# Optimization experiments

Measured on AMD Instinct MI355X. Metric: run time of the kernel, lower is better.

Reference implementation:

```python
import jax, jax.numpy as jnp
import numpy as np

N_NODES = 20000
N_EDGES = 50000
IN_DIM = 128
HID = 128
OUT_DIM = 64
N_PAIRS = 128
N_LAYERS = 2
N_HEADS = 4


def setup_inputs() -> dict:
    key = jax.random.key(0)
    ks = jax.random.split(key, 32)
    s = 0.05
    def p(k, shape):
        return jax.random.normal(k, shape, jnp.float32) * s
    inp = {}
    inp["node_features"] = jax.random.normal(ks[0], (N_NODES, IN_DIM), jnp.float32)
    inp["edge_index"] = jax.random.randint(ks[1], (2, N_EDGES), 0, N_NODES, jnp.int32)
    inp["edge_timestamps"] = jax.random.uniform(ks[2], (N_EDGES,), jnp.float32)
    inp["target_pairs"] = jax.random.randint(ks[3], (N_PAIRS, 2), 0, N_NODES, jnp.int32)
    inp["in_W"] = p(ks[4], (HID, IN_DIM)); inp["in_b"] = p(ks[5], (HID,))
    inp["te_W1"] = p(ks[6], (N_LAYERS, HID, 1)); inp["te_b1"] = p(ks[7], (N_LAYERS, HID))
    inp["te_W2"] = p(ks[8], (N_LAYERS, HID, HID)); inp["te_b2"] = p(ks[9], (N_LAYERS, HID))
    inp["attn_in_W"] = p(ks[10], (N_LAYERS, 3 * HID, HID)); inp["attn_in_b"] = p(ks[11], (N_LAYERS, 3 * HID))
    inp["attn_out_W"] = p(ks[12], (N_LAYERS, HID, HID)); inp["attn_out_b"] = p(ks[13], (N_LAYERS, HID))
    inp["ft_W"] = p(ks[14], (N_LAYERS, HID, HID)); inp["ft_b"] = p(ks[15], (N_LAYERS, HID))
    inp["op_W"] = p(ks[16], (N_LAYERS, HID, HID)); inp["op_b"] = p(ks[17], (N_LAYERS, HID))
    inp["out1_W"] = p(ks[18], (HID, HID)); inp["out1_b"] = p(ks[19], (HID,))
    inp["out2_W"] = p(ks[20], (OUT_DIM, HID)); inp["out2_b"] = p(ks[21], (OUT_DIM,))
    inp["lp1_W"] = p(ks[22], (HID, 2 * OUT_DIM)); inp["lp1_b"] = p(ks[23], (HID,))
    inp["lp2_W"] = p(ks[24], (HID // 2, HID)); inp["lp2_b"] = p(ks[25], (HID // 2,))
    inp["lp3_W"] = p(ks[26], (1, HID // 2)); inp["lp3_b"] = p(ks[27], (1,))
    return inp


def _forward(node_features, edge_index, edge_timestamps, target_pairs,
             in_W, in_b, te_W1, te_b1, te_W2, te_b2,
             attn_in_W, attn_in_b, attn_out_W, attn_out_b,
             ft_W, ft_b, op_W, op_b,
             out1_W, out1_b, out2_W, out2_b,
             lp1_W, lp1_b, lp2_W, lp2_b, lp3_W, lp3_b):
    N = node_features.shape[0]
    h = in_W.shape[0]
    H = N_HEADS
    d = h // H
    scale = 1.0 / np.sqrt(d).astype(np.float32)
    src, dst = edge_index[0], edge_index[1]
    # flattened target nodes; duplicates compute identical rows so dedup (torch.unique) is unneeded
    targets = target_pairs.reshape(-1)  # [U]
    U = targets.shape[0]
    E = src.shape[0]

    x = node_features @ in_W.T + in_b  # [N, h]
    for l in range(te_W1.shape[0]):
        tf = x @ ft_W[l].T + ft_b[l]                                           # [N, h]
        tfeat = jax.nn.relu(edge_timestamps[:, None] @ te_W1[l].T + te_b1[l])
        tfeat = tfeat @ te_W2[l].T + te_b2[l]                                  # [E, h]
        Wq, Wk, Wv = jnp.split(attn_in_W[l], 3, axis=0)
        bq, bk, bv = jnp.split(attn_in_b[l], 3)
        q = (tf[targets] @ Wq.T + bq).reshape(U, H, d)
        # keys/values are linear in (tf[nbr] + tfeat): split into node term A and edge term B
        Ak = (tf @ Wk.T).reshape(N, H, d)
        Bk = (tfeat @ Wk.T + bk).reshape(E, H, d)
        Av = (tf @ Wv.T).reshape(N, H, d)
        Bv = (tfeat @ Wv.T + bv).reshape(E, H, d)
        is_src = src[None, :] == targets[:, None]          # [U, E]
        mask = is_src | (dst[None, :] == targets[:, None])  # edge incident to target
        nbr = jnp.where(is_src, dst[None, :], src[None, :])  # other endpoint, [U, E]
        qAk = jnp.einsum('uhd,nhd->uhn', q, Ak) * scale      # [U, H, N]
        idx = jnp.broadcast_to(nbr[:, None, :], (U, H, E))
        s_node = jnp.take_along_axis(qAk, idx, axis=2)        # [U, H, E]
        s_edge = jnp.einsum('uhd,ehd->uhe', q, Bk) * scale
        scores = jnp.where(mask[:, None, :], s_node + s_edge, -1e30)
        p = jax.nn.softmax(scores, axis=-1)
        p = jnp.where(mask[:, None, :], p, 0.0)               # [U, H, E]
        out_edge = jnp.einsum('uhe,ehd->uhd', p, Bv)
        # sum_e p * Av[nbr] via per-target scatter of probs into node space
        w = jax.vmap(lambda pe, ne: jax.ops.segment_sum(pe, ne, num_segments=N))(
            p.transpose(0, 2, 1), nbr)                        # [U, N, H]
        out_node = jnp.einsum('unh,nhd->uhd', w, Av)
        attn = (out_node + out_edge).reshape(U, h) @ attn_out_W[l].T + attn_out_b[l]
        has_nbr = mask.any(axis=1)
        agg_in = jnp.where(has_nbr[:, None], attn, tf[targets])
        agg = agg_in @ op_W[l].T + op_b[l]
        x = x.at[targets].set(agg)
        x = jax.nn.relu(x)
    emb = jax.nn.relu(x @ out1_W.T + out1_b) @ out2_W.T + out2_b  # [N, out]
    pair = jnp.concatenate([emb[target_pairs[:, 0]], emb[target_pairs[:, 1]]], axis=1)
    z = jax.nn.relu(pair @ lp1_W.T + lp1_b)
    z = jax.nn.relu(z @ lp2_W.T + lp2_b)
    return jax.nn.sigmoid(z @ lp3_W.T + lp3_b)  # [B, 1]


def reference(node_features, edge_index, edge_timestamps, target_pairs,
              in_W, in_b, te_W1, te_b1, te_W2, te_b2,
              attn_in_W, attn_in_b, attn_out_W, attn_out_b,
              ft_W, ft_b, op_W, op_b,
              out1_W, out1_b, out2_W, out2_b,
              lp1_W, lp1_b, lp2_W, lp2_b, lp3_W, lp3_b):
    return _forward(node_features, edge_index, edge_timestamps, target_pairs,
                    in_W, in_b, te_W1, te_b1, te_W2, te_b2,
                    attn_in_W, attn_in_b, attn_out_W, attn_out_b,
                    ft_W, ft_b, op_W, op_b,
                    out1_W, out1_b, out2_W, out2_b,
                    lp1_W, lp1_b, lp2_W, lp2_b, lp3_W, lp3_b)
```

## Files before the change

kernel.cpp:

```cpp
#include <hip/hip_runtime.h>
#include <math.h>

#define N_NODES 20000
#define N_EDGES 50000
#define N_SLOTS 256
#define N_PAIRS 128
#define CAP 32
#define MSTRIDE 16384
#define NMAT 19
#define TFLAG (1 << 30)
#define HSZ 1024
#define NBLK 256
#define BATCH 16

__device__ __forceinline__ float4 relu4(float4 v) {
    return make_float4(fmaxf(v.x, 0.f), fmaxf(v.y, 0.f), fmaxf(v.z, 0.f), fmaxf(v.w, 0.f));
}
__device__ __forceinline__ float4 add4(float4 a, float4 b) {
    return make_float4(a.x + b.x, a.y + b.y, a.z + b.z, a.w + b.w);
}
__device__ __forceinline__ void fma4(float4& acc, const float4 w, const float s) {
    acc.x = fmaf(w.x, s, acc.x); acc.y = fmaf(w.y, s, acc.y);
    acc.z = fmaf(w.z, s, acc.z); acc.w = fmaf(w.w, s, acc.w);
}
#define F4Z make_float4(0.f, 0.f, 0.f, 0.f)

__device__ __forceinline__ void gbar(unsigned* cnt, unsigned target, bool wait) {
    __syncthreads();
    if (threadIdx.x == 0) {
        __builtin_amdgcn_fence(__ATOMIC_RELEASE, "agent");
        __hip_atomic_fetch_add(cnt, 1u, __ATOMIC_RELAXED, __HIP_MEMORY_SCOPE_AGENT);
        if (wait) {
            int it = 0;
            while (true) {
                unsigned v;
                if ((it++ & 7) != 7)
                    v = __hip_atomic_load(cnt, __ATOMIC_RELAXED,
                                          __HIP_MEMORY_SCOPE_SYSTEM);
                else
                    v = __hip_atomic_fetch_add(cnt, 0u, __ATOMIC_RELAXED,
                                               __HIP_MEMORY_SCOPE_AGENT);
                if (v >= target) break;
                __builtin_amdgcn_s_sleep(16);
            }
            __builtin_amdgcn_fence(__ATOMIC_ACQUIRE, "agent");
        }
    }
    __syncthreads();
}

__device__ __forceinline__ float4 mv_ks1_g8(const float* __restrict__ WT,
                                            const float* __restrict__ xv128,
                                            int g, int jj) {
    const float4* W4 = (const float4*)WT;
    const float4* x4 = (const float4*)xv128;
    float4 acc = F4Z;
#pragma unroll
    for (int kk4 = 0; kk4 < 4; ++kk4) {
        int k4 = g * 4 + kk4;
        float4 xv = x4[k4];
        fma4(acc, W4[(k4 * 4 + 0) * 32 + jj], xv.x);
        fma4(acc, W4[(k4 * 4 + 1) * 32 + jj], xv.y);
        fma4(acc, W4[(k4 * 4 + 2) * 32 + jj], xv.z);
        fma4(acc, W4[(k4 * 4 + 3) * 32 + jj], xv.w);
    }
    return acc;
}
__device__ __forceinline__ float4 mv_ks1_g8_64(const float* __restrict__ WT,
                                               const float* __restrict__ xv128,
                                               int g, int jj) {
    const float4* W4 = (const float4*)WT;
    const float4* x4 = (const float4*)xv128;
    int j16 = jj & 15;
    float4 acc = F4Z;
#pragma unroll
    for (int kk4 = 0; kk4 < 4; ++kk4) {
        int k4 = g * 4 + kk4;
        float4 xv = x4[k4];
        fma4(acc, W4[(k4 * 4 + 0) * 16 + j16], xv.x);
        fma4(acc, W4[(k4 * 4 + 1) * 16 + j16], xv.y);
        fma4(acc, W4[(k4 * 4 + 2) * 16 + j16], xv.z);
        fma4(acc, W4[(k4 * 4 + 3) * 16 + j16], xv.w);
    }
    return acc;
}
__device__ __forceinline__ float4 comb1_g8(const float4* pb, int jj) {
    float4 s = pb[jj];
#pragma unroll
    for (int gp = 1; gp < 8; ++gp) s = add4(s, pb[gp * 32 + jj]);
    return s;
}

__device__ __forceinline__ void mv16_g8(const float* __restrict__ WT,
                                        const float* __restrict__ xs,
                                        int g, int jj, float4* acc) {
    const float4* W4 = (const float4*)WT;
    const float4* x4 = (const float4*)xs;
#pragma unroll
    for (int kk4 = 0; kk4 < 4; ++kk4) {
        int k4 = g * 4 + kk4;
        float4 w0 = W4[(k4 * 4 + 0) * 32 + jj];
        float4 w1 = W4[(k4 * 4 + 1) * 32 + jj];
        float4 w2 = W4[(k4 * 4 + 2) * 32 + jj];
        float4 w3 = W4[(k4 * 4 + 3) * 32 + jj];
#pragma unroll
        for (int e = 0; e < 16; ++e) {
            float4 xv = x4[e * 32 + k4];
            fma4(acc[e], w0, xv.x); fma4(acc[e], w1, xv.y);
            fma4(acc[e], w2, xv.z); fma4(acc[e], w3, xv.w);
        }
    }
}
__device__ __forceinline__ float4 comb16_g8(const float4* pb, int it, int jj) {
    float4 s = pb[it * 32 + jj];
#pragma unroll
    for (int gp = 1; gp < 8; ++gp) s = add4(s, pb[(gp * 16 + it) * 32 + jj]);
    return s;
}

__device__ __forceinline__ float4 mv_ks1(const float* __restrict__ WT,
                                         const float* __restrict__ xv128,
                                         int g, int jj) {
    const float4* W4 = (const float4*)WT;
    const float4* x4 = (const float4*)xv128;
    float4 acc = F4Z;
#pragma unroll 2
    for (int kk4 = 0; kk4 < 8; ++kk4) {
        int k4 = g * 8 + kk4;
        float4 xv = x4[k4];
        fma4(acc, W4[(k4 * 4 + 0) * 32 + jj], xv.x);
        fma4(acc, W4[(k4 * 4 + 1) * 32 + jj], xv.y);
        fma4(acc, W4[(k4 * 4 + 2) * 32 + jj], xv.z);
        fma4(acc, W4[(k4 * 4 + 3) * 32 + jj], xv.w);
    }
    return acc;
}
__device__ __forceinline__ float4 mv_ks1_64(const float* __restrict__ WT,
                                            const float* __restrict__ xv128,
                                            int g, int jj) {
    const float4* W4 = (const float4*)WT;
    const float4* x4 = (const float4*)xv128;
    int j16 = jj & 15;
    float4 acc = F4Z;
#pragma unroll 2
    for (int kk4 = 0; kk4 < 8; ++kk4) {
        int k4 = g * 8 + kk4;
        float4 xv = x4[k4];
        fma4(acc, W4[(k4 * 4 + 0) * 16 + j16], xv.x);
        fma4(acc, W4[(k4 * 4 + 1) * 16 + j16], xv.y);
        fma4(acc, W4[(k4 * 4 + 2) * 16 + j16], xv.z);
        fma4(acc, W4[(k4 * 4 + 3) * 16 + j16], xv.w);
    }
    return acc;
}
__device__ __forceinline__ float4 comb1(const float4* pb, int jj) {
    return add4(add4(pb[jj], pb[32 + jj]), add4(pb[64 + jj], pb[96 + jj]));
}

__device__ __forceinline__ unsigned thash(int key) {
    return ((unsigned)key * 2654435761u) >> 22;
}
__device__ __forceinline__ bool hexists(const int* __restrict__ hkey, int key) {
    unsigned h = thash(key);
    while (true) {
        int k = hkey[h];
        if (k == -1) return false;
        if (k == key) return true;
        h = (h + 1) & (HSZ - 1);
    }
}
__device__ __forceinline__ void hemit_g(const int* __restrict__ hkey,
                                        const int* __restrict__ hval,
                                        int* __restrict__ gcnt,
                                        int2* __restrict__ lst,
                                        int key, int e, int nbrf) {
    unsigned h = thash(key);
    while (true) {
        int k = hkey[h];
        if (k == -1) return;
        if (k == key) {
            int s = hval[h];
            int pos = atomicAdd(&gcnt[s], 1);
            if (pos < CAP) lst[s * CAP + pos] = make_int2(e, nbrf);
        }
        h = (h + 1) & (HSZ - 1);
    }
}

struct Params {
    const float* nf; const int* ei; const float* ts; const int* tp;
    const float* inW; const float* inb;
    const float* teW1; const float* teb1; const float* teW2; const float* teb2;
    const float* aiW; const float* aib; const float* aoW; const float* aob;
    const float* ftW; const float* ftb; const float* opW; const float* opb;
    const float* o1W; const float* o1b; const float* o2W; const float* o2b;
    const float* l1W; const float* l1b; const float* l2W; const float* l2b;
    const float* l3W; const float* l3b;
    float* out; float* x; int* cnt; int2* lst; float* emb; float* WT;
    unsigned* bar; unsigned* flg;
};

__global__ __launch_bounds__(256, 1) void k_fused(Params P) {
    __shared__ __align__(16) float xu[128], x0u[128], tfv[128], qv[128], sv[128];
    __shared__ __align__(16) float xs[BATCH * 128], t1s[BATCH * 128];
    __shared__ __align__(16) float x0s[BATCH * 128];
    __shared__ __align__(16) float zs[CAP * 128];
    __shared__ __align__(16) float4 pb[8 * 16 * 32];
    __shared__ __align__(16) float qkh[4 * 128];
    __shared__ __align__(16) float zbl[4 * 128];
    __shared__ float scl[CAP * 4], ps[CAP * 4], sbk[4];
    __shared__ int nbr_s[BATCH], tf_s[BATCH];
    __shared__ float ts_s[BATCH];
    __shared__ __align__(16) float tile[32][129];
    __shared__ int hkey[HSZ], hval[HSZ];

    const int b = blockIdx.x, tid = threadIdx.x, g = tid >> 5, jj = tid & 31;

    if (b < 72) {
        int m, r0, rows;
        if (b < 68) { m = b >> 2; r0 = (b & 3) * 32; rows = 128; }
        else { int mm = b - 68; m = 17 + (mm >> 1); r0 = (mm & 1) * 32; rows = 64; }
        const float* src;
        if (m == 0) src = P.inW;
        else if (m <= 2) src = P.ftW + (m - 1) * MSTRIDE;
        else if (m <= 4) src = P.teW2 + (m - 3) * MSTRIDE;
        else if (m <= 10) src = P.aiW + (m - 5) * MSTRIDE;
        else if (m <= 12) src = P.aoW + (m - 11) * MSTRIDE;
        else if (m <= 14) src = P.opW + (m - 13) * MSTRIDE;
        else if (m == 15) src = P.o1W;
        else if (m == 16) src = P.l1W;
        else if (m == 17) src = P.o2W;
        else src = P.l2W;
        float* dst = P.WT + m * MSTRIDE;
        for (int idx = tid; idx < 32 * 128; idx += 256) {
            int r = idx >> 7, cc = idx & 127;
            tile[r][cc] = src[(r0 + r) * 128 + cc];
        }
        __syncthreads();
        for (int idx = tid; idx < 128 * 32; idx += 256) {
            int k = idx >> 5, jr = idx & 31;
            dst[k * rows + r0 + jr] = tile[jr][k];
        }
    } else {
        for (int i = tid; i < HSZ; i += 256) hkey[i] = -1;
        __syncthreads();
        {
            int uu = P.tp[tid];
            unsigned h = thash(uu);
            while (atomicCAS(&hkey[h], -1, uu) != -1) h = (h + 1) & (HSZ - 1);
            hval[h] = tid;
        }
        __syncthreads();
        const int4* s4 = (const int4*)P.ei;
        const int4* d4 = (const int4*)(P.ei + N_EDGES);
        const int NE4 = N_EDGES / 4;
        const int nscan = NBLK - 72;
        const int chunk = (NE4 + nscan - 1) / nscan;
        const int start = (b - 72) * chunk;
        const int end = min(start + chunk, NE4);
        for (int e4 = start + tid; e4 < end; e4 += 256) {
            int4 s = s4[e4];
            int4 d = d4[e4];
            int ss[4] = {s.x, s.y, s.z, s.w};
            int dd[4] = {d.x, d.y, d.z, d.w};
#pragma unroll
            for (int t = 0; t < 4; ++t) {
                int a = ss[t], bb = dd[t];
                bool atgt = hexists(hkey, a);
                bool btgt = (bb == a) ? atgt : hexists(hkey, bb);
                if (!atgt && !btgt) continue;
                int e = e4 * 4 + t;
                if (atgt) hemit_g(hkey, hval, P.cnt, P.lst, a, e, bb | (btgt ? TFLAG : 0));
                if (btgt && bb != a) hemit_g(hkey, hval, P.cnt, P.lst, bb, e, a | (atgt ? TFLAG : 0));
            }
        }
    }
    gbar(P.bar, NBLK, true);

    const float scale = 0.17677669529663687f;
    const int u = P.tp[b];
    const int c = min(P.cnt[b], CAP);

    for (int layer = 0; layer < 2; ++layer) {
        const float* WT_in = P.WT;
        const float* WT_ft = P.WT + (1 + layer) * MSTRIDE;
        const float* WT_te2 = P.WT + (3 + layer) * MSTRIDE;
        const float* WT_q = P.WT + (5 + 3 * layer) * MSTRIDE;
        const float* WT_v = P.WT + (7 + 3 * layer) * MSTRIDE;
        const float* WT_ao = P.WT + (11 + layer) * MSTRIDE;
        const float* WT_op = P.WT + (13 + layer) * MSTRIDE;
        const float* inb = P.inb;
        const float* ftb = P.ftb + layer * 128;
        const float* teW1 = P.teW1 + layer * 128;
        const float* teb1 = P.teb1 + layer * 128;
        const float* teb2 = P.teb2 + layer * 128;
        const float* bq = P.aib + layer * 384;
        const float* bk = bq + 128;
        const float* bv = bq + 256;
        const float* aob = P.aob + layer * 128;
        const float* opb = P.opb + layer * 128;

        if (tid < 128) xu[tid] = (layer == 0) ? P.nf[(size_t)u * 128 + tid]
                                              : P.x[(size_t)u * 128 + tid];
        __syncthreads();
        const float* xeff = xu;
        if (layer == 0) {
            pb[g * 32 + jj] = mv_ks1_g8(WT_in, xu, g, jj);
            __syncthreads();
            if (g == 0)
                *(float4*)(x0u + jj * 4) = add4(comb1_g8(pb, jj), *(const float4*)(inb + jj * 4));
            xeff = x0u;
            __syncthreads();
        }
        pb[g * 32 + jj] = mv_ks1_g8(WT_ft, xeff, g, jj);
        __syncthreads();
        if (g == 0)
            *(float4*)(tfv + jj * 4) = add4(comb1_g8(pb, jj), *(const float4*)(ftb + jj * 4));
        __syncthreads();
        pb[g * 32 + jj] = mv_ks1_g8(WT_q, tfv, g, jj);
        __syncthreads();
        if (g == 0)
            *(float4*)(qv + jj * 4) = add4(comb1_g8(pb, jj), *(const float4*)(bq + jj * 4));
        __syncthreads();
        {
            const float* WkRaw = P.aiW + (size_t)layer * 3 * MSTRIDE + MSTRIDE;
            int i = tid & 127, hb = tid >> 7;
#pragma unroll
            for (int s = 0; s < 2; ++s) {
                int h = hb * 2 + s;
                float a = 0.f;
#pragma unroll 8
                for (int j = 0; j < 32; ++j)
                    a = fmaf(WkRaw[(size_t)(h * 32 + j) * 128 + i], qv[h * 32 + j], a);
                qkh[h * 128 + i] = a;
            }
            if (tid < 128) {
                float pp = qv[tid] * bk[tid];
                pp += __shfl_xor(pp, 1, 32); pp += __shfl_xor(pp, 2, 32);
                pp += __shfl_xor(pp, 4, 32); pp += __shfl_xor(pp, 8, 32);
                pp += __shfl_xor(pp, 16, 32);
                if ((tid & 31) == 0) sbk[tid >> 5] = pp;
            }
        }
        __syncthreads();

        for (int base = 0; base < c; base += BATCH) {
            if (tid < BATCH) {
                int i = base + tid;
                int2 en = (i < c) ? P.lst[b * CAP + i] : make_int2(0, 0);
                nbr_s[tid] = en.y & ~TFLAG;
                tf_s[tid] = (en.y & TFLAG) ? 1 : 0;
                ts_s[tid] = (i < c) ? P.ts[en.x] : 0.f;
            }
            __syncthreads();
            {
                int c0 = jj * 4;
                float4 w = *(const float4*)(teW1 + c0);
                float4 bb = *(const float4*)(teb1 + c0);
#pragma unroll
                for (int s = 0; s < 2; ++s) {
                    int e = g + s * 8;
                    const float* srcp = (layer == 0) ? (P.nf + (size_t)nbr_s[e] * 128 + c0)
                                                     : (P.x + (size_t)nbr_s[e] * 128 + c0);
                    float4 v = *(const float4*)srcp;
                    float* dstp = (layer == 0) ? xs : x0s;
                    *(float4*)(dstp + e * 128 + c0) = v;
                    float tse = ts_s[e];
                    *(float4*)(t1s + e * 128 + c0) =
                        make_float4(fmaxf(fmaf(tse, w.x, bb.x), 0.f),
                                    fmaxf(fmaf(tse, w.y, bb.y), 0.f),
                                    fmaxf(fmaf(tse, w.z, bb.z), 0.f),
                                    fmaxf(fmaf(tse, w.w, bb.w), 0.f));
                }
            }
            __syncthreads();
            if (layer == 0) {
                float4 acc[16] = {F4Z, F4Z, F4Z, F4Z, F4Z, F4Z, F4Z, F4Z,
                                  F4Z, F4Z, F4Z, F4Z, F4Z, F4Z, F4Z, F4Z};
                mv16_g8(WT_in, xs, g, jj, acc);
#pragma unroll
                for (int e = 0; e < 16; ++e) pb[(g * 16 + e) * 32 + jj] = acc[e];
                __syncthreads();
#pragma unroll
                for (int s = 0; s < 2; ++s) {
                    int it = 2 * g + s;
                    float4 x0v = add4(comb16_g8(pb, it, jj), *(const float4*)(inb + jj * 4));
                    *(float4*)(x0s + it * 128 + jj * 4) = x0v;
                    if (base + it < c && !tf_s[it])
                        *(float4*)(P.x + (size_t)nbr_s[it] * 128 + jj * 4) = relu4(x0v);
                }
                __syncthreads();
            }
            {
                float4 acc[16] = {F4Z, F4Z, F4Z, F4Z, F4Z, F4Z, F4Z, F4Z,
                                  F4Z, F4Z, F4Z, F4Z, F4Z, F4Z, F4Z, F4Z};
                mv16_g8(WT_ft, x0s, g, jj, acc);
                mv16_g8(WT_te2, t1s, g, jj, acc);
#pragma unroll
                for (int e = 0; e < 16; ++e) pb[(g * 16 + e) * 32 + jj] = acc[e];
                __syncthreads();
                float4 zb4 = add4(*(const float4*)(ftb + jj * 4),
                                  *(const float4*)(teb2 + jj * 4));
#pragma unroll
                for (int s = 0; s < 2; ++s) {
                    int it = 2 * g + s;
                    *(float4*)(zs + (size_t)(base + it) * 128 + jj * 4) =
                        add4(comb16_g8(pb, it, jj), zb4);
                }
                __syncthreads();
            }
            {
                int it = tid >> 4, l = tid & 15, item = base + it;
                const float* zp = zs + (size_t)item * 128;
                float s0 = 0.f, s1 = 0.f, s2 = 0.f, s3 = 0.f;
#pragma unroll
                for (int dd = 0; dd < 8; ++dd) {
                    int d = dd * 16 + l;
                    float zv = zp[d];
                    s0 = fmaf(qkh[d], zv, s0);
                    s1 = fmaf(qkh[128 + d], zv, s1);
                    s2 = fmaf(qkh[256 + d], zv, s2);
                    s3 = fmaf(qkh[384 + d], zv, s3);
                }
                s0 += __shfl_xor(s0, 1, 16); s0 += __shfl_xor(s0, 2, 16);
                s0 += __shfl_xor(s0, 4, 16); s0 += __shfl_xor(s0, 8, 16);
                s1 += __shfl_xor(s1, 1, 16); s1 += __shfl_xor(s1, 2, 16);
                s1 += __shfl_xor(s1, 4, 16); s1 += __shfl_xor(s1, 8, 16);
                s2 += __shfl_xor(s2, 1, 16); s2 += __shfl_xor(s2, 2, 16);
                s2 += __shfl_xor(s2, 4, 16); s2 += __shfl_xor(s2, 8, 16);
                s3 += __shfl_xor(s3, 1, 16); s3 += __shfl_xor(s3, 2, 16);
                s3 += __shfl_xor(s3, 4, 16); s3 += __shfl_xor(s3, 8, 16);
                if (l == 0 && item < c) {
                    scl[item * 4 + 0] = (s0 + sbk[0]) * scale;
                    scl[item * 4 + 1] = (s1 + sbk[1]) * scale;
                    scl[item * 4 + 2] = (s2 + sbk[2]) * scale;
                    scl[item * 4 + 3] = (s3 + sbk[3]) * scale;
                }
                __syncthreads();
            }
        }

        if (tid < 128 && c > 0) {
            int hd = tid >> 5, e = tid & 31;
            float m = -INFINITY;
            for (int i = 0; i < c; ++i) m = fmaxf(m, scl[i * 4 + hd]);
            float l = 0.f;
            for (int i = 0; i < c; ++i) l += __expf(scl[i * 4 + hd] - m);
            if (e < c) ps[e * 4 + hd] = __expf(scl[e * 4 + hd] - m) / l;
        }
        __syncthreads();
        {
            int i = tid & 127, hb = tid >> 7;
#pragma unroll
            for (int s = 0; s < 2; ++s) {
                int h = hb * 2 + s;
                float a = 0.f;
                for (int e = 0; e < c; ++e)
                    a = fmaf(ps[e * 4 + h], zs[(size_t)e * 128 + i], a);
                zbl[h * 128 + i] = a;
            }
        }
        __syncthreads();
        pb[g * 32 + jj] = mv_ks1_g8(WT_v, zbl + (jj >> 3) * 128, g, jj);
        __syncthreads();
        if (g == 0) {
            float4 vv = add4(comb1_g8(pb, jj), *(const float4*)(bv + jj * 4));
            if (c == 0) vv = F4Z;
            *(float4*)(sv + jj * 4) = vv;
        }
        __syncthreads();
        pb[g * 32 + jj] = mv_ks1_g8(WT_ao, sv, g, jj);
        __syncthreads();
        if (g == 0) {
            float4 z4;
            if (c > 0) z4 = add4(comb1_g8(pb, jj), *(const float4*)(aob + jj * 4));
            else z4 = *(const float4*)(tfv + jj * 4);
            *(float4*)(xu + jj * 4) = z4;
        }
        __syncthreads();
        pb[g * 32 + jj] = mv_ks1_g8(WT_op, xu, g, jj);
        __syncthreads();
        if (layer == 0) {
            if (g == 0) {
                float4 a = relu4(add4(comb1_g8(pb, jj), *(const float4*)(opb + jj * 4)));
                *(float4*)(P.x + (size_t)u * 128 + jj * 4) = a;
            }
            gbar(P.bar, NBLK * 2, true);
        } else {
            if (g == 0)
                *(float4*)(x0u + jj * 4) =
                    relu4(add4(comb1_g8(pb, jj), *(const float4*)(opb + jj * 4)));
            __syncthreads();
            pb[g * 32 + jj] = mv_ks1_g8(P.WT + 15 * MSTRIDE, x0u, g, jj);
            __syncthreads();
            if (g == 0)
                *(float4*)(tfv + jj * 4) =
                    relu4(add4(comb1_g8(pb, jj), *(const float4*)(P.o1b + jj * 4)));
            __syncthreads();
            pb[g * 32 + jj] = mv_ks1_g8_64(P.WT + 17 * MSTRIDE, tfv, g, jj);
            __syncthreads();
            if (g == 0 && jj < 16)
                *(float4*)(P.emb + (size_t)b * 64 + jj * 4) =
                    add4(comb1_g8(pb, jj), *(const float4*)(P.o2b + jj * 4));
            __syncthreads();
            if (tid == 0) {
                __builtin_amdgcn_fence(__ATOMIC_RELEASE, "agent");
                __hip_atomic_store(&P.flg[b], 1u, __ATOMIC_RELAXED,
                                   __HIP_MEMORY_SCOPE_AGENT);
            }
        }
    }

    if (b < N_PAIRS) {
        if (tid == 0) {
            while (__hip_atomic_load(&P.flg[2 * b], __ATOMIC_RELAXED,
                                     __HIP_MEMORY_SCOPE_SYSTEM) == 0u ||
                   __hip_atomic_load(&P.flg[2 * b + 1], __ATOMIC_RELAXED,
                                     __HIP_MEMORY_SCOPE_SYSTEM) == 0u)
                __builtin_amdgcn_s_sleep(4);
            __builtin_amdgcn_fence(__ATOMIC_ACQUIRE, "agent");
        }
        __syncthreads();
        const float* WT_l1 = P.WT + 16 * MSTRIDE;
        const float* WT_l2 = P.WT + 18 * MSTRIDE;
        if (tid < 128)
            xu[tid] = (tid < 64) ? P.emb[(size_t)(2 * b) * 64 + tid]
                                 : P.emb[(size_t)(2 * b + 1) * 64 + (tid - 64)];
        __syncthreads();
        if (tid < 128) pb[g * 32 + jj] = mv_ks1(WT_l1, xu, g, jj);
        __syncthreads();
        if (tid < 128 && g == 0)
            *(float4*)(tfv + jj * 4) =
                relu4(add4(comb1(pb, jj), *(const float4*)(P.l1b + jj * 4)));
        __syncthreads();
        if (tid < 128) pb[g * 32 + jj] = mv_ks1_64(WT_l2, tfv, g, jj);
        __syncthreads();
        if (tid < 128 && g == 0 && jj < 16)
            *(float4*)(qv + jj * 4) =
                relu4(add4(comb1(pb, jj), *(const float4*)(P.l2b + jj * 4)));
        __syncthreads();
        if (tid < 64) {
            float v = qv[tid] * P.l3W[tid];
            v += __shfl_xor(v, 1);
            v += __shfl_xor(v, 2);
            v += __shfl_xor(v, 4);
            v += __shfl_xor(v, 8);
            v += __shfl_xor(v, 16);
            v += __shfl_xor(v, 32);
            if (tid == 0) P.out[b] = 1.f / (1.f + __expf(-(v + P.l3b[0])));
        }
    }
}

extern "C" void kernel_launch(void* const* d_in, const int* in_sizes, int n_in,
                              void* d_out, int out_size, void* d_ws, size_t ws_size,
                              hipStream_t stream) {
    Params P;
    P.nf  = (const float*)d_in[0];
    P.ei  = (const int*)d_in[1];
    P.ts  = (const float*)d_in[2];
    P.tp  = (const int*)d_in[3];
    P.inW = (const float*)d_in[4];
    P.inb = (const float*)d_in[5];
    P.teW1 = (const float*)d_in[6];
    P.teb1 = (const float*)d_in[7];
    P.teW2 = (const float*)d_in[8];
    P.teb2 = (const float*)d_in[9];
    P.aiW = (const float*)d_in[10];
    P.aib = (const float*)d_in[11];
    P.aoW = (const float*)d_in[12];
    P.aob = (const float*)d_in[13];
    P.ftW = (const float*)d_in[14];
    P.ftb = (const float*)d_in[15];
    P.opW = (const float*)d_in[16];
    P.opb = (const float*)d_in[17];
    P.o1W = (const float*)d_in[18];
    P.o1b = (const float*)d_in[19];
    P.o2W = (const float*)d_in[20];
    P.o2b = (const float*)d_in[21];
    P.l1W = (const float*)d_in[22];
    P.l1b = (const float*)d_in[23];
    P.l2W = (const float*)d_in[24];
    P.l2b = (const float*)d_in[25];
    P.l3W = (const float*)d_in[26];
    P.l3b = (const float*)d_in[27];
    P.out = (float*)d_out;

    char* ws = (char*)d_ws;
    size_t off = 0;
    P.x    = (float*)(ws + off); off += (size_t)N_NODES * 128 * 4;
    P.cnt  = (int*)  (ws + off); off += N_SLOTS * 4;
    P.lst  = (int2*) (ws + off); off += (size_t)N_SLOTS * CAP * 8;
    P.emb  = (float*)(ws + off); off += N_SLOTS * 64 * 4;
    P.WT   = (float*)(ws + off); off += (size_t)NMAT * MSTRIDE * 4;
    P.bar  = (unsigned*)(ws + off); off += 4;
    P.flg  = (unsigned*)(ws + off); off += N_SLOTS * 4;

    hipMemsetAsync(P.cnt, 0, N_SLOTS * 4, stream);
    hipMemsetAsync(P.bar, 0, 4 + N_SLOTS * 4, stream);
    k_fused<<<NBLK, 256, 0, stream>>>(P);
}
```

Before: 199.5 us.

## Pre-multiply consecutive linear layers into fused weight matrices in spare blocks

Blocks 232-255 no longer scan edges. They compute fused matrices ftW·inW and opW·aoW, plus their fused biases, during the prologue. The per-target chain then replaces two back-to-back matvecs with one in layer 0 input/ft and in the attention-out/op stage, removing two matvec+sync rounds per layer. In exchange, edge scanning moves onto fewer blocks and the prologue does extra 128x128x128 matmul work, which may lengthen the phase before the first grid barrier.

```diff
diff --git a/kernel.cpp b/kernel.cpp
--- a/kernel.cpp
+++ b/kernel.cpp
@@ -7,11 +7,12 @@
 #define N_PAIRS 128
 #define CAP 32
 #define MSTRIDE 16384
-#define NMAT 19
+#define NMAT 22
 #define TFLAG (1 << 30)
 #define HSZ 1024
 #define NBLK 256
 #define BATCH 16
+#define NSCAN_END 232
 
 __device__ __forceinline__ float4 relu4(float4 v) {
     return make_float4(fmaxf(v.x, 0.f), fmaxf(v.y, 0.f), fmaxf(v.z, 0.f), fmaxf(v.w, 0.f));
@@ -197,7 +198,7 @@
     const float* l1W; const float* l1b; const float* l2W; const float* l2b;
     const float* l3W; const float* l3b;
     float* out; float* x; int* cnt; int2* lst; float* emb; float* WT;
-    unsigned* bar; unsigned* flg;
+    unsigned* bar; unsigned* flg; float* bfus;
 };
 
 __global__ __launch_bounds__(256, 1) void k_fused(Params P) {
@@ -241,7 +242,7 @@
             int k = idx >> 5, jr = idx & 31;
             dst[k * rows + r0 + jr] = tile[jr][k];
         }
-    } else {
+    } else if (b < NSCAN_END) {
         for (int i = tid; i < HSZ; i += 256) hkey[i] = -1;
         __syncthreads();
         {
@@ -254,7 +255,7 @@
         const int4* s4 = (const int4*)P.ei;
         const int4* d4 = (const int4*)(P.ei + N_EDGES);
         const int NE4 = N_EDGES / 4;
-        const int nscan = NBLK - 72;
+        const int nscan = NSCAN_END - 72;
         const int chunk = (NE4 + nscan - 1) / nscan;
         const int start = (b - 72) * chunk;
         const int end = min(start + chunk, NE4);
@@ -274,6 +275,41 @@
                 if (btgt && bb != a) hemit_g(hkey, hval, P.cnt, P.lst, bb, e, a | (atgt ? TFLAG : 0));
             }
         }
+    } else {
+        int fb = b - NSCAN_END, mid = fb >> 3, sub = fb & 7;
+        const float *A, *B, *bvec, *cvec;
+        float *MT, *bout;
+        if (mid == 0) {
+            A = P.ftW; B = P.inW; bvec = P.inb; cvec = P.ftb;
+            MT = P.WT + 19 * MSTRIDE; bout = P.bfus;
+        } else {
+            int l = mid - 1;
+            A = P.opW + (size_t)l * MSTRIDE; B = P.aoW + (size_t)l * MSTRIDE;
+            bvec = P.aob + l * 128; cvec = P.opb + l * 128;
+            MT = P.WT + (20 + l) * MSTRIDE; bout = P.bfus + (1 + l) * 128;
+        }
+        float* Bl = (float*)pb;
+        for (int i = tid; i < 4096; i += 256)
+            ((float4*)Bl)[i] = ((const float4*)B)[i];
+        __syncthreads();
+#pragma unroll
+        for (int rr = 0; rr < 8; ++rr) {
+            int j = sub * 16 + rr * 2 + (tid >> 7);
+            int k = tid & 127;
+            const float* Aj = A + (size_t)j * 128;
+            float acc = 0.f;
+#pragma unroll 8
+            for (int m = 0; m < 128; ++m)
+                acc = fmaf(Aj[m], Bl[m * 128 + k], acc);
+            MT[(size_t)k * 128 + j] = acc;
+        }
+        if (tid < 16) {
+            int j = sub * 16 + tid;
+            const float* Aj = A + (size_t)j * 128;
+            float s = 0.f;
+            for (int m = 0; m < 128; ++m) s = fmaf(Aj[m], bvec[m], s);
+            bout[j] = s + cvec[j];
+        }
     }
     gbar(P.bar, NBLK, true);
 
@@ -287,7 +323,6 @@
         const float* WT_te2 = P.WT + (3 + layer) * MSTRIDE;
         const float* WT_q = P.WT + (5 + 3 * layer) * MSTRIDE;
         const float* WT_v = P.WT + (7 + 3 * layer) * MSTRIDE;
-        const float* WT_ao = P.WT + (11 + layer) * MSTRIDE;
         const float* WT_op = P.WT + (13 + layer) * MSTRIDE;
         const float* inb = P.inb;
         const float* ftb = P.ftb + layer * 128;
@@ -297,26 +332,20 @@
         const float* bq = P.aib + layer * 384;
         const float* bk = bq + 128;
         const float* bv = bq + 256;
-        const float* aob = P.aob + layer * 128;
         const float* opb = P.opb + layer * 128;
 
         if (tid < 128) xu[tid] = (layer == 0) ? P.nf[(size_t)u * 128 + tid]
                                               : P.x[(size_t)u * 128 + tid];
         __syncthreads();
-        const float* xeff = xu;
-        if (layer == 0) {
-            pb[g * 32 + jj] = mv_ks1_g8(WT_in, xu, g, jj);
+        {
+            const float* Wt = (layer == 0) ? (P.WT + 19 * MSTRIDE) : WT_ft;
+            const float* bt = (layer == 0) ? P.bfus : ftb;
+            pb[g * 32 + jj] = mv_ks1_g8(Wt, xu, g, jj);
             __syncthreads();
             if (g == 0)
-                *(float4*)(x0u + jj * 4) = add4(comb1_g8(pb, jj), *(const float4*)(inb + jj * 4));
-            xeff = x0u;
-            __syncthreads();
-        }
-        pb[g * 32 + jj] = mv_ks1_g8(WT_ft, xeff, g, jj);
-        __syncthreads();
-        if (g == 0)
-            *(float4*)(tfv + jj * 4) = add4(comb1_g8(pb, jj), *(const float4*)(ftb + jj * 4));
-        __syncthreads();
+                *(float4*)(tfv + jj * 4) = add4(comb1_g8(pb, jj), *(const float4*)(bt + jj * 4));
+            __syncthreads();
+        }
         pb[g * 32 + jj] = mv_ks1_g8(WT_q, tfv, g, jj);
         __syncthreads();
         if (g == 0)
@@ -469,27 +498,23 @@
             *(float4*)(sv + jj * 4) = vv;
         }
         __syncthreads();
-        pb[g * 32 + jj] = mv_ks1_g8(WT_ao, sv, g, jj);
-        __syncthreads();
-        if (g == 0) {
-            float4 z4;
-            if (c > 0) z4 = add4(comb1_g8(pb, jj), *(const float4*)(aob + jj * 4));
-            else z4 = *(const float4*)(tfv + jj * 4);
-            *(float4*)(xu + jj * 4) = z4;
-        }
-        __syncthreads();
-        pb[g * 32 + jj] = mv_ks1_g8(WT_op, xu, g, jj);
-        __syncthreads();
+        {
+            const float* Wf = (c > 0) ? (P.WT + (20 + layer) * MSTRIDE) : WT_op;
+            const float* xf = (c > 0) ? sv : tfv;
+            const float* bf = (c > 0) ? (P.bfus + (1 + layer) * 128) : opb;
+            pb[g * 32 + jj] = mv_ks1_g8(Wf, xf, g, jj);
+            __syncthreads();
+            if (g == 0) {
+                float4 a = relu4(add4(comb1_g8(pb, jj), *(const float4*)(bf + jj * 4)));
+                if (layer == 0)
+                    *(float4*)(P.x + (size_t)u * 128 + jj * 4) = a;
+                else
+                    *(float4*)(x0u + jj * 4) = a;
+            }
+        }
         if (layer == 0) {
-            if (g == 0) {
-                float4 a = relu4(add4(comb1_g8(pb, jj), *(const float4*)(opb + jj * 4)));
-                *(float4*)(P.x + (size_t)u * 128 + jj * 4) = a;
-            }
             gbar(P.bar, NBLK * 2, true);
         } else {
-            if (g == 0)
-                *(float4*)(x0u + jj * 4) =
-                    relu4(add4(comb1_g8(pb, jj), *(const float4*)(opb + jj * 4)));
             __syncthreads();
             pb[g * 32 + jj] = mv_ks1_g8(P.WT + 15 * MSTRIDE, x0u, g, jj);
             __syncthreads();
@@ -593,10 +618,11 @@
     P.lst  = (int2*) (ws + off); off += (size_t)N_SLOTS * CAP * 8;
     P.emb  = (float*)(ws + off); off += N_SLOTS * 64 * 4;
     P.WT   = (float*)(ws + off); off += (size_t)NMAT * MSTRIDE * 4;
-    P.bar  = (unsigned*)(ws + off); off += 4;
+    P.bar  = (unsigned*)(ws + off); off += 16;
     P.flg  = (unsigned*)(ws + off); off += N_SLOTS * 4;
+    P.bfus = (float*)(ws + off); off += 3 * 128 * 4;
 
     hipMemsetAsync(P.cnt, 0, N_SLOTS * 4, stream);
-    hipMemsetAsync(P.bar, 0, 4 + N_SLOTS * 4, stream);
+    hipMemsetAsync(P.bar, 0, 16 + N_SLOTS * 4, stream);
     k_fused<<<NBLK, 256, 0, stream>>>(P);
 }
```

After: 222.8 us. 1.12x slower.
